# Kernel tuning notes

Measured on AMD Instinct MI355X. Metric: run time of the kernel, lower is better.

## Reference

```python
import jax, jax.numpy as jnp
import numpy as np

B, R, C, H = 2048, 100, 64, 256  # batch graphs, regions/graph, in_channels, hidden
N = B * R                         # total nodes
E = 3276800                       # edges


def setup_inputs() -> dict:
    key = jax.random.key(0)
    ks = jax.random.split(key, 12)
    state = jax.random.normal(ks[0], (N, C), dtype=jnp.float32)
    edge_index = jax.random.randint(ks[1], (2, E), 0, N, dtype=jnp.int64)
    action = jax.random.uniform(ks[2], (B, R, R), dtype=jnp.float32)
    s = lambda f: 1.0 / np.sqrt(f)
    W_gcn = jax.random.uniform(ks[3], (C, C), jnp.float32, -s(C), s(C))
    b_gcn = jnp.zeros((C,), jnp.float32)
    W1 = jax.random.uniform(ks[4], (C + R, H), jnp.float32, -s(C + R), s(C + R))
    b1 = jax.random.uniform(ks[5], (H,), jnp.float32, -s(C + R), s(C + R))
    W2 = jax.random.uniform(ks[6], (H, H), jnp.float32, -s(H), s(H))
    b2 = jax.random.uniform(ks[7], (H,), jnp.float32, -s(H), s(H))
    W3 = jax.random.uniform(ks[8], (H, 1), jnp.float32, -s(H), s(H))
    b3 = jax.random.uniform(ks[9], (1,), jnp.float32, -s(H), s(H))
    return {"state": state, "edge_index": edge_index, "action": action,
            "W_gcn": W_gcn, "b_gcn": b_gcn, "W1": W1, "b1": b1,
            "W2": W2, "b2": b2, "W3": W3, "b3": b3}


def gcn_conv(x, edge_index, W, b):
    # PyG GCNConv: add self-loops, symmetric degree normalization, then aggregate.
    n = x.shape[0]
    loops = jnp.arange(n, dtype=edge_index.dtype)
    src = jnp.concatenate([edge_index[0], loops])
    dst = jnp.concatenate([edge_index[1], loops])
    deg = jax.ops.segment_sum(jnp.ones_like(dst, dtype=x.dtype), dst, num_segments=n)
    dinv = deg ** -0.5  # deg >= 1 thanks to self-loops
    xw = x @ W
    msg = xw[src] * (dinv[src] * dinv[dst])[:, None]
    return jax.ops.segment_sum(msg, dst, num_segments=n) + b


def reference(state, edge_index, action, W_gcn, b_gcn, W1, b1, W2, b2, W3, b3):
    out = jax.nn.relu(gcn_conv(state, edge_index, W_gcn, b_gcn))
    x = out + state                              # residual, [N, C]
    x = x.reshape(-1, R, C)                      # [B, R, C]
    concat = jnp.concatenate([x, action], axis=-1)  # [B, R, C+R]
    x = jax.nn.relu(concat @ W1 + b1)
    x = jax.nn.relu(x @ W2 + b2)
    x = jnp.sum(x, axis=1)                       # sum pooling over regions -> [B, H]
    return (x @ W3 + b3).squeeze(-1)             # [B]
```

## Files before the change

### kernel.cpp

```cpp
#include <hip/hip_runtime.h>
#include <hip/hip_bf16.h>
#include <cstdint>
#include <cstddef>

#define N_NODES 204800
#define N_EDGES 3276800
#define NB 2048
#define NR 100
#define NC 64
#define NH 256
#define KPAD 192
#define NBKT 400
#define H1P 264

typedef __attribute__((ext_vector_type(8))) short short8;
typedef __attribute__((ext_vector_type(4))) float f32x4;
typedef unsigned int uint32;

__device__ __forceinline__ void gload16(const void* g, void* l) {
    __builtin_amdgcn_global_load_lds(
        (const __attribute__((address_space(1))) uint32_t*)(g),
        (__attribute__((address_space(3))) uint32_t*)(l), 16, 0, 0);
}

__device__ __forceinline__ ushort f2bf(float v) {
    __hip_bfloat16 h = __float2bfloat16(v);
    return *reinterpret_cast<ushort*>(&h);
}

__device__ __forceinline__ uint32 pack2bf(float a, float b) {
    return (uint32)f2bf(a) | ((uint32)f2bf(b) << 16);
}

__device__ __forceinline__ float bflo(uint32 v) { return __uint_as_float(v << 16); }
__device__ __forceinline__ float bfhi(uint32 v) { return __uint_as_float(v & 0xFFFF0000u); }


__global__ __launch_bounds__(256) void k_bhist(const int* __restrict__ ei,
                                               int* __restrict__ bcnt) {
    __shared__ int h[NBKT];
    int t = threadIdx.x;
    for (int i = t; i < NBKT; i += 256) h[i] = 0;
    __syncthreads();
    #pragma unroll 8
    for (int k = 0; k < 8; ++k) {
        int e = blockIdx.x * 2048 + k * 256 + t;
        atomicAdd(&h[ei[N_EDGES + e] >> 9], 1);
    }
    __syncthreads();
    for (int i = t; i < NBKT; i += 256)
        if (h[i]) atomicAdd(&bcnt[i], h[i]);
}

__global__ void k_bscan(const int* __restrict__ bcnt, int* __restrict__ boffs,
                        int* __restrict__ bcur) {
    __shared__ int tmp[512];
    int t = threadIdx.x;
    int v = (t < NBKT) ? bcnt[t] : 0;
    tmp[t] = v;
    __syncthreads();
    for (int off = 1; off < 512; off <<= 1) {
        int x = 0;
        if (t >= off) x = tmp[t - off];
        __syncthreads();
        tmp[t] += x;
        __syncthreads();
    }
    if (t < NBKT) {
        int o = tmp[t] - v;
        boffs[t] = o;
        bcur[t] = o;
    }
}

__global__ __launch_bounds__(256) void k_bscat(const int* __restrict__ ei,
                                               int* __restrict__ bcur,
                                               uint32* __restrict__ part) {
    __shared__ int hist[NBKT];
    int tid = threadIdx.x;
    for (int i = tid; i < NBKT; i += 256) hist[i] = 0;
    __syncthreads();

    uint32 w[8];
    int bk[8], r[8];
    #pragma unroll 8
    for (int k = 0; k < 8; ++k) {
        int e = blockIdx.x * 2048 + k * 256 + tid;
        int s = ei[e];
        int d = ei[N_EDGES + e];
        int b = d >> 9;
        w[k] = (uint32)s | ((uint32)(d & 511) << 18);
        bk[k] = b;
        r[k] = atomicAdd(&hist[b], 1);
    }
    __syncthreads();
    for (int i = tid; i < NBKT; i += 256) {
        int c = hist[i];
        hist[i] = c ? atomicAdd(&bcur[i], c) : 0;
    }
    __syncthreads();
    #pragma unroll 8
    for (int k = 0; k < 8; ++k)
        part[hist[bk[k]] + r[k]] = w[k];
}

__global__ __launch_bounds__(512) void k_sortb(
    const uint32* __restrict__ part, const int* __restrict__ boffs,
    const int* __restrict__ bcnt, int* __restrict__ csr,
    int* __restrict__ cnt, int* __restrict__ offs, float* __restrict__ dinv) {
    __shared__ int h[512];
    __shared__ int cur[512];
    int b = blockIdx.x, t = threadIdx.x;
    h[t] = 0;
    __syncthreads();
    int base = boffs[b], n = bcnt[b];
    for (int i = t; i < n; i += 512)
        atomicAdd(&h[part[base + i] >> 18], 1);
    __syncthreads();
    int v = h[t];
    int node = b * 512 + t;
    cnt[node] = v;
    dinv[node] = rsqrtf((float)(v + 1));
    __syncthreads();
    for (int off = 1; off < 512; off <<= 1) {
        int x = 0;
        if (t >= off) x = h[t - off];
        __syncthreads();
        h[t] += x;
        __syncthreads();
    }
    int excl = h[t] - v;
    offs[node] = base + excl;
    cur[t] = excl;
    __syncthreads();
    for (int i = t; i < n; i += 512) {
        uint32 ew = part[base + i];
        int dl = ew >> 18;
        int pos = atomicAdd(&cur[dl], 1);
        csr[base + pos] = (int)(ew & 0x3FFFF);
    }
}

__global__ void k_ssb(const float* __restrict__ state, const float* __restrict__ dinv,
                      uint32* __restrict__ ssb32) {
    int idx = blockIdx.x * 256 + threadIdx.x;
    int row = idx >> 5;
    float d = dinv[row];
    float2 v = reinterpret_cast<const float2*>(state)[idx];
    ssb32[idx] = pack2bf(v.x * d, v.y * d);
}

__global__ __launch_bounds__(256) void k_gcn(
    const uint32* __restrict__ ssb32, const float* __restrict__ state,
    const int* __restrict__ csr, const int* __restrict__ offs,
    const int* __restrict__ cnt, const float* __restrict__ dinv,
    const ushort* __restrict__ Wgt, const float* __restrict__ bg,
    ushort* __restrict__ xb16) {
    __shared__ uint32 av[32 * 36];
    __shared__ ushort wgs[64 * 72];
    int tid = threadIdx.x;
    int w = tid >> 6, lane = tid & 63;
    int half = lane >> 5, l = lane & 31;
    int R0 = blockIdx.x * 32;

    {
        int r = tid >> 2, c0 = (tid & 3) * 16;
        short8 v0 = *(const short8*)(Wgt + r * 64 + c0);
        short8 v1 = *(const short8*)(Wgt + r * 64 + c0 + 8);
        *(short8*)(wgs + r * 72 + c0) = v0;
        *(short8*)(wgs + r * 72 + c0 + 8) = v1;
    }

    for (int rr = 0; rr < 4; ++rr) {
        int lrow = w * 8 + rr * 2 + half;
        int row = R0 + lrow;
        float di = dinv[row];
        float2 st2 = *reinterpret_cast<const float2*>(state + (size_t)row * 64 + 2 * l);
        int s0 = offs[row], c = cnt[row];
        float x0 = 0.f, y0 = 0.f, x1 = 0.f, y1 = 0.f;
        float x2 = 0.f, y2 = 0.f, x3 = 0.f, y3 = 0.f;
        int e = 0;
        for (; e + 8 <= c; e += 8) {
            int sa = csr[s0 + e + 0];
            int sb = csr[s0 + e + 1];
            int sc = csr[s0 + e + 2];
            int sd = csr[s0 + e + 3];
            int se = csr[s0 + e + 4];
            int sf = csr[s0 + e + 5];
            int sg = csr[s0 + e + 6];
            int sh = csr[s0 + e + 7];
            uint32 va = ssb32[(size_t)sa * 32 + l];
            uint32 vb = ssb32[(size_t)sb * 32 + l];
            uint32 vc = ssb32[(size_t)sc * 32 + l];
            uint32 vd = ssb32[(size_t)sd * 32 + l];
            uint32 ve = ssb32[(size_t)se * 32 + l];
            uint32 vf = ssb32[(size_t)sf * 32 + l];
            uint32 vg = ssb32[(size_t)sg * 32 + l];
            uint32 vh = ssb32[(size_t)sh * 32 + l];
            x0 += bflo(va); y0 += bfhi(va);
            x1 += bflo(vb); y1 += bfhi(vb);
            x2 += bflo(vc); y2 += bfhi(vc);
            x3 += bflo(vd); y3 += bfhi(vd);
            x0 += bflo(ve); y0 += bfhi(ve);
            x1 += bflo(vf); y1 += bfhi(vf);
            x2 += bflo(vg); y2 += bfhi(vg);
            x3 += bflo(vh); y3 += bfhi(vh);
        }
        for (; e + 4 <= c; e += 4) {
            int sa = csr[s0 + e + 0];
            int sb = csr[s0 + e + 1];
            int sc = csr[s0 + e + 2];
            int sd = csr[s0 + e + 3];
            uint32 va = ssb32[(size_t)sa * 32 + l];
            uint32 vb = ssb32[(size_t)sb * 32 + l];
            uint32 vc = ssb32[(size_t)sc * 32 + l];
            uint32 vd = ssb32[(size_t)sd * 32 + l];
            x0 += bflo(va); y0 += bfhi(va);
            x1 += bflo(vb); y1 += bfhi(vb);
            x2 += bflo(vc); y2 += bfhi(vc);
            x3 += bflo(vd); y3 += bfhi(vd);
        }
        for (; e < c; ++e) {
            int s = csr[s0 + e];
            uint32 v = ssb32[(size_t)s * 32 + l];
            x0 += bflo(v); y0 += bfhi(v);
        }
        float ax = ((x0 + x1) + (x2 + x3)) * di + di * di * st2.x;
        float ay = ((y0 + y1) + (y2 + y3)) * di + di * di * st2.y;
        av[lrow * 36 + l] = pack2bf(ax, ay);
    }
    __syncthreads();

    int l15 = lane & 15, l4 = lane >> 4;
    const ushort* avs = (const ushort*)av;
    f32x4 acc[2] = {};
    #pragma unroll
    for (int kk = 0; kk < 2; ++kk) {
        short8 bf = *(const short8*)(wgs + (w * 16 + l15) * 72 + kk * 32 + l4 * 8);
        #pragma unroll
        for (int mt = 0; mt < 2; ++mt) {
            short8 af = *(const short8*)(avs + (mt * 16 + l15) * 72 + kk * 32 + l4 * 8);
            acc[mt] = __builtin_amdgcn_mfma_f32_16x16x32_bf16(af, bf, acc[mt], 0, 0, 0);
        }
    }
    int col = w * 16 + l15;
    float bgv = bg[col];
    #pragma unroll
    for (int mt = 0; mt < 2; ++mt)
        #pragma unroll
        for (int r = 0; r < 4; ++r) {
            int row = R0 + mt * 16 + l4 * 4 + r;
            float v = fmaxf(acc[mt][r] + bgv, 0.f) + state[(size_t)row * 64 + col];
            xb16[(size_t)row * 64 + col] = f2bf(v);
        }
}

__global__ void k_packW(const float* __restrict__ W1, const float* __restrict__ W2,
                        const float* __restrict__ Wg, ushort* __restrict__ W1f,
                        ushort* __restrict__ W2f, ushort* __restrict__ Wgt) {
    int t = blockIdx.x * 256 + threadIdx.x;
    if (t < 6 * 4 * 256 * 8) {
        int u = t & 7, chunk = t >> 3;
        int tid = chunk & 255, ktI = chunk >> 8;
        int kt = ktI >> 2, i = ktI & 3;
        int l = tid & 63, wp = tid >> 6;
        int k = kt * 32 + (l >> 4) * 8 + u;
        int j = i * 64 + wp * 16 + (l & 15);
        W1f[t] = (k < NC + NR) ? f2bf(W1[(size_t)k * NH + j]) : (ushort)0;
    } else if (t < 49152 + 8 * 4 * 256 * 8) {
        int t2 = t - 49152;
        int u = t2 & 7, chunk = t2 >> 3;
        int tid = chunk & 255, ktI = chunk >> 8;
        int kt = ktI >> 2, i = ktI & 3;
        int l = tid & 63, wp = tid >> 6;
        int k = kt * 32 + (l >> 4) * 8 + u;
        int j = i * 64 + wp * 16 + (l & 15);
        W2f[t2] = f2bf(W2[(size_t)k * NH + j]);
    } else {
        int t3 = t - 49152 - 65536;
        if (t3 < 64 * 64) {
            int n = t3 >> 6, k = t3 & 63;
            Wgt[t3] = f2bf(Wg[(size_t)k * 64 + n]);
        }
    }
}

__global__ __launch_bounds__(256, 2) void k_mlpf(
    const ushort* __restrict__ xb16, const float* __restrict__ action,
    const ushort* __restrict__ W1f, const ushort* __restrict__ W2f,
    const float* __restrict__ b1, const float* __restrict__ b2,
    const float* __restrict__ W3, float* __restrict__ out) {
    __shared__ __align__(16) ushort As[2][64 * 32];
    __shared__ __align__(16) ushort Bs[2][256 * 32];
    __shared__ __align__(16) ushort H1s[64 * H1P];
    int tid = threadIdx.x;
    int w = tid >> 6, lane = tid & 63;
    int m0 = blockIdx.x * 64;
    int l15 = lane & 15, l4 = lane >> 4;

    int arow = (tid >> 6) * 16 + (tid & 15);
    int aseg = (tid >> 4) & 3;
    int gr = m0 + arow;
    int gb = gr / 100, grr = gr - gb * 100;
    const float* abp = action + (size_t)gb * 10000 + (size_t)grr * 100;

    float b1v[4], b2v[4], w3v[4];
    #pragma unroll
    for (int nt = 0; nt < 4; ++nt) {
        int col = w * 64 + nt * 16 + l15;
        b1v[nt] = b1[col];
        b2v[nt] = b2[col];
        w3v[nt] = W3[col];
    }

    f32x4 acc[4][4] = {};

    #pragma unroll
    for (int i = 0; i < 4; ++i)
        gload16(W1f + ((size_t)(0 * 4 + i) * 256 + tid) * 8, (char*)Bs[0] + i * 4096 + tid * 16);
    gload16(xb16 + (size_t)gr * 64 + 0 * 32 + aseg * 8, (char*)As[0] + tid * 16);
    __syncthreads();

    int cur = 0;
    for (int kt = 0; kt < 6; ++kt) {
        int nxt = cur ^ 1;
        if (kt < 5) {
            #pragma unroll
            for (int i = 0; i < 4; ++i)
                gload16(W1f + ((size_t)((kt + 1) * 4 + i) * 256 + tid) * 8,
                        (char*)Bs[nxt] + i * 4096 + tid * 16);
            if (kt + 1 < 2) {
                gload16(xb16 + (size_t)gr * 64 + (kt + 1) * 32 + aseg * 8,
                        (char*)As[nxt] + tid * 16);
            } else {
                int c0 = (kt + 1) * 32 - 64 + aseg * 8;
                ushort tmp[8];
                #pragma unroll
                for (int u = 0; u < 8; ++u) {
                    int cc = c0 + u;
                    tmp[u] = (cc < NR) ? f2bf(abp[cc]) : (ushort)0;
                }
                *(short8*)((char*)As[nxt] + tid * 16) = *(const short8*)tmp;
            }
        } else {
            #pragma unroll
            for (int i = 0; i < 4; ++i)
                gload16(W2f + ((size_t)(0 * 4 + i) * 256 + tid) * 8,
                        (char*)Bs[nxt] + i * 4096 + tid * 16);
        }
        short8 af[4], bf[4];
        #pragma unroll
        for (int mt = 0; mt < 4; ++mt)
            af[mt] = *(const short8*)((const char*)As[cur] + mt * 1024 + lane * 16);
        #pragma unroll
        for (int nt = 0; nt < 4; ++nt)
            bf[nt] = *(const short8*)((const char*)Bs[cur] + w * 4096 + nt * 1024 + lane * 16);
        #pragma unroll
        for (int mt = 0; mt < 4; ++mt)
            #pragma unroll
            for (int nt = 0; nt < 4; ++nt)
                acc[mt][nt] = __builtin_amdgcn_mfma_f32_16x16x32_bf16(
                    af[mt], bf[nt], acc[mt][nt], 0, 0, 0);
        if (kt == 5) {
            #pragma unroll
            for (int mt = 0; mt < 4; ++mt)
                #pragma unroll
                for (int nt = 0; nt < 4; ++nt) {
                    int col = w * 64 + nt * 16 + l15;
                    #pragma unroll
                    for (int r = 0; r < 4; ++r) {
                        int row = mt * 16 + l4 * 4 + r;
                        H1s[row * H1P + col] = f2bf(fmaxf(acc[mt][nt][r] + b1v[nt], 0.f));
                    }
                }
        }
        __syncthreads();
        cur = nxt;
    }

    #pragma unroll
    for (int mt = 0; mt < 4; ++mt)
        #pragma unroll
        for (int nt = 0; nt < 4; ++nt)
            acc[mt][nt] = (f32x4){0.f, 0.f, 0.f, 0.f};

    for (int kt = 0; kt < 8; ++kt) {
        int nxt = cur ^ 1;
        if (kt < 7) {
            #pragma unroll
            for (int i = 0; i < 4; ++i)
                gload16(W2f + ((size_t)((kt + 1) * 4 + i) * 256 + tid) * 8,
                        (char*)Bs[nxt] + i * 4096 + tid * 16);
        }
        int k0 = kt * 32;
        short8 af[4], bf[4];
        #pragma unroll
        for (int mt = 0; mt < 4; ++mt)
            af[mt] = *(const short8*)((const char*)H1s +
                     ((size_t)(mt * 16 + l15) * H1P + k0 + l4 * 8) * 2);
        #pragma unroll
        for (int nt = 0; nt < 4; ++nt)
            bf[nt] = *(const short8*)((const char*)Bs[cur] + w * 4096 + nt * 1024 + lane * 16);
        #pragma unroll
        for (int mt = 0; mt < 4; ++mt)
            #pragma unroll
            for (int nt = 0; nt < 4; ++nt)
                acc[mt][nt] = __builtin_amdgcn_mfma_f32_16x16x32_bf16(
                    af[mt], bf[nt], acc[mt][nt], 0, 0, 0);
        __syncthreads();
        cur = nxt;
    }

    float* red = (float*)As;
    #pragma unroll
    for (int mt = 0; mt < 4; ++mt)
        #pragma unroll
        for (int r = 0; r < 4; ++r) {
            float v = 0.f;
            #pragma unroll
            for (int nt = 0; nt < 4; ++nt)
                v += fmaxf(acc[mt][nt][r] + b2v[nt], 0.f) * w3v[nt];
            v += __shfl_xor(v, 1);
            v += __shfl_xor(v, 2);
            v += __shfl_xor(v, 4);
            v += __shfl_xor(v, 8);
            if (l15 == 0) red[(mt * 16 + l4 * 4 + r) * 4 + w] = v;
        }
    __syncthreads();
    if (tid < 64) {
        float s = red[tid * 4 + 0] + red[tid * 4 + 1] + red[tid * 4 + 2] + red[tid * 4 + 3];
        int gbase = m0;
        int g0 = gbase / 100;
        int r0 = gbase - g0 * 100;
        int split = 100 - r0; if (split > 64) split = 64;
        float v0 = (tid < split) ? s : 0.f;
        float vs = s;
        #pragma unroll
        for (int d = 1; d < 64; d <<= 1) {
            v0 += __shfl_xor(v0, d);
            vs += __shfl_xor(vs, d);
        }
        if (tid == 0) {
            atomicAdd(&out[g0], v0);
            if (split < 64) atomicAdd(&out[g0 + 1], vs - v0);
        }
    }
}

__global__ void k_init_out(float* __restrict__ out, const float* __restrict__ b3) {
    int i = blockIdx.x * 256 + threadIdx.x;
    out[i] = b3[0];
}


extern "C" void kernel_launch(void* const* d_in, const int* in_sizes, int n_in,
                              void* d_out, int out_size, void* d_ws, size_t ws_size,
                              hipStream_t stream) {
    const float* state  = (const float*)d_in[0];
    const int*   ei     = (const int*)d_in[1];
    const float* action = (const float*)d_in[2];
    const float* Wg     = (const float*)d_in[3];
    const float* bg     = (const float*)d_in[4];
    const float* W1     = (const float*)d_in[5];
    const float* b1     = (const float*)d_in[6];
    const float* W2     = (const float*)d_in[7];
    const float* b2     = (const float*)d_in[8];
    const float* W3     = (const float*)d_in[9];
    const float* b3     = (const float*)d_in[10];
    float* out = (float*)d_out;

    char* ws = (char*)d_ws;
    uint32* part  = (uint32*)(ws + 0);
    uint32* ssb32 = (uint32*)(ws + 13107200);
    ushort* xb16  = (ushort*)(ws + 39321600);
    int*   csr    = (int*)  (ws + 65536000);
    int*   cnt    = (int*)  (ws + 78643200);
    int*   offs   = (int*)  (ws + 79462400);
    float* dinv   = (float*)(ws + 80281600);
    int*   bcnt   = (int*)  (ws + 81100800);
    int*   boffs  = (int*)  (ws + 81102400);
    int*   bcur   = (int*)  (ws + 81104000);
    ushort* W1f   = (ushort*)(ws + 81105600);
    ushort* W2f   = (ushort*)(ws + 81203904);
    ushort* Wgt   = (ushort*)(ws + 81334976);

    hipMemsetAsync(bcnt, 0, NBKT * sizeof(int), stream);
    k_init_out<<<NB / 256, 256, 0, stream>>>(out, b3);

    k_bhist<<<N_EDGES / 2048, 256, 0, stream>>>(ei, bcnt);
    k_bscan<<<1, 512, 0, stream>>>(bcnt, boffs, bcur);
    k_bscat<<<N_EDGES / 2048, 256, 0, stream>>>(ei, bcur, part);
    k_sortb<<<NBKT, 512, 0, stream>>>(part, boffs, bcnt, csr, cnt, offs, dinv);
    k_ssb<<<(N_NODES * 32) / 256, 256, 0, stream>>>(state, dinv, ssb32);
    k_packW<<<(49152 + 65536 + 4096 + 255) / 256, 256, 0, stream>>>(
        W1, W2, Wg, W1f, W2f, Wgt);
    k_gcn<<<N_NODES / 32, 256, 0, stream>>>(ssb32, state, csr, offs, cnt, dinv,
                                            Wgt, bg, xb16);
    k_mlpf<<<N_NODES / 64, 256, 0, stream>>>(xb16, action, W1f, W2f, b1, b2, W3, out);
}
```

Before: 324.7 us.

## Restructure fused MLP to keep activations in registers and fold b1 into W1

Reworks the fused MLP kernel so each wave owns 16 rows and all 256 output columns. It computes a transposed first layer with the row data as the B operand, keeps H1 in registers, and rebuilds the layer-2 A fragments with lane shuffles instead of an LDS H1 buffer. Bias b1 is folded into the packed W1 as an extra K row driven by a constant 1.0 input, and action values are loaded as float4 vectors. Dropping the As/H1s shared buffers cuts LDS so occupancy can rise to 3 blocks, at the cost of higher register pressure (two 16-tile accumulator arrays) and extra shuffle work.

```diff
diff --git a/kernel.cpp b/kernel.cpp
--- a/kernel.cpp
+++ b/kernel.cpp
@@ -11,7 +11,6 @@
 #define NH 256
 #define KPAD 192
 #define NBKT 400
-#define H1P 264
 
 typedef __attribute__((ext_vector_type(8))) short short8;
 typedef __attribute__((ext_vector_type(4))) float f32x4;
@@ -256,8 +255,9 @@
 }
 
 __global__ void k_packW(const float* __restrict__ W1, const float* __restrict__ W2,
-                        const float* __restrict__ Wg, ushort* __restrict__ W1f,
-                        ushort* __restrict__ W2f, ushort* __restrict__ Wgt) {
+                        const float* __restrict__ Wg, const float* __restrict__ b1,
+                        ushort* __restrict__ W1f, ushort* __restrict__ W2f,
+                        ushort* __restrict__ Wgt) {
     int t = blockIdx.x * 256 + threadIdx.x;
     if (t < 6 * 4 * 256 * 8) {
         int u = t & 7, chunk = t >> 3;
@@ -266,7 +266,10 @@
         int l = tid & 63, wp = tid >> 6;
         int k = kt * 32 + (l >> 4) * 8 + u;
         int j = i * 64 + wp * 16 + (l & 15);
-        W1f[t] = (k < NC + NR) ? f2bf(W1[(size_t)k * NH + j]) : (ushort)0;
+        ushort v = 0;
+        if (k < NC + NR) v = f2bf(W1[(size_t)k * NH + j]);
+        else if (k == NC + NR) v = f2bf(b1[j]);
+        W1f[t] = v;
     } else if (t < 49152 + 8 * 4 * 256 * 8) {
         int t2 = t - 49152;
         int u = t2 & 7, chunk = t2 >> 3;
@@ -285,105 +288,95 @@
     }
 }
 
-__global__ __launch_bounds__(256, 2) void k_mlpf(
+__global__ __launch_bounds__(256, 3) void k_mlpf(
     const ushort* __restrict__ xb16, const float* __restrict__ action,
     const ushort* __restrict__ W1f, const ushort* __restrict__ W2f,
-    const float* __restrict__ b1, const float* __restrict__ b2,
-    const float* __restrict__ W3, float* __restrict__ out) {
-    __shared__ __align__(16) ushort As[2][64 * 32];
+    const float* __restrict__ b2, const float* __restrict__ W3,
+    float* __restrict__ out) {
     __shared__ __align__(16) ushort Bs[2][256 * 32];
-    __shared__ __align__(16) ushort H1s[64 * H1P];
     int tid = threadIdx.x;
     int w = tid >> 6, lane = tid & 63;
+    int s = lane & 15, g = lane >> 4;
     int m0 = blockIdx.x * 64;
-    int l15 = lane & 15, l4 = lane >> 4;
-
-    int arow = (tid >> 6) * 16 + (tid & 15);
-    int aseg = (tid >> 4) & 3;
-    int gr = m0 + arow;
-    int gb = gr / 100, grr = gr - gb * 100;
+    int myrow = m0 + w * 16 + s;
+    int gb = myrow / 100, grr = myrow - gb * 100;
     const float* abp = action + (size_t)gb * 10000 + (size_t)grr * 100;
 
-    float b1v[4], b2v[4], w3v[4];
-    #pragma unroll
-    for (int nt = 0; nt < 4; ++nt) {
-        int col = w * 64 + nt * 16 + l15;
-        b1v[nt] = b1[col];
-        b2v[nt] = b2[col];
-        w3v[nt] = W3[col];
-    }
-
-    f32x4 acc[4][4] = {};
+    short8 xf0 = *(const short8*)(xb16 + (size_t)myrow * 64 + g * 8);
+    short8 xf1 = *(const short8*)(xb16 + (size_t)myrow * 64 + 32 + g * 8);
 
     #pragma unroll
     for (int i = 0; i < 4; ++i)
-        gload16(W1f + ((size_t)(0 * 4 + i) * 256 + tid) * 8, (char*)Bs[0] + i * 4096 + tid * 16);
-    gload16(xb16 + (size_t)gr * 64 + 0 * 32 + aseg * 8, (char*)As[0] + tid * 16);
-    __syncthreads();
-
+        gload16(W1f + ((size_t)(0 * 4 + i) * 256 + tid) * 8,
+                (char*)Bs[0] + i * 4096 + tid * 16);
+    __syncthreads();
+
+    f32x4 acc1[16] = {};
+    float4 pa0 = {0.f, 0.f, 0.f, 0.f}, pa1 = {0.f, 0.f, 0.f, 0.f};
     int cur = 0;
+
+    #pragma unroll
     for (int kt = 0; kt < 6; ++kt) {
         int nxt = cur ^ 1;
+        short8 bf;
+        if (kt == 0) bf = xf0;
+        else if (kt == 1) bf = xf1;
+        else if (kt < 5) {
+            ushort tm[8];
+            tm[0] = f2bf(pa0.x); tm[1] = f2bf(pa0.y); tm[2] = f2bf(pa0.z); tm[3] = f2bf(pa0.w);
+            tm[4] = f2bf(pa1.x); tm[5] = f2bf(pa1.y); tm[6] = f2bf(pa1.z); tm[7] = f2bf(pa1.w);
+            bf = *(const short8*)tm;
+        } else {
+            ushort tm[8];
+            if (g == 0) {
+                tm[0] = f2bf(pa0.x); tm[1] = f2bf(pa0.y); tm[2] = f2bf(pa0.z); tm[3] = f2bf(pa0.w);
+                tm[4] = (ushort)0x3F80; tm[5] = 0; tm[6] = 0; tm[7] = 0;
+            } else {
+                #pragma unroll
+                for (int u = 0; u < 8; ++u) tm[u] = 0;
+            }
+            bf = *(const short8*)tm;
+        }
+        if (kt >= 1 && kt <= 3) {
+            int c0 = (kt + 1) * 32 - 64 + g * 8;
+            pa0 = *(const float4*)(abp + c0);
+            pa1 = *(const float4*)(abp + c0 + 4);
+        } else if (kt == 4) {
+            if (g == 0) pa0 = *(const float4*)(abp + 96);
+        }
         if (kt < 5) {
             #pragma unroll
             for (int i = 0; i < 4; ++i)
                 gload16(W1f + ((size_t)((kt + 1) * 4 + i) * 256 + tid) * 8,
                         (char*)Bs[nxt] + i * 4096 + tid * 16);
-            if (kt + 1 < 2) {
-                gload16(xb16 + (size_t)gr * 64 + (kt + 1) * 32 + aseg * 8,
-                        (char*)As[nxt] + tid * 16);
-            } else {
-                int c0 = (kt + 1) * 32 - 64 + aseg * 8;
-                ushort tmp[8];
-                #pragma unroll
-                for (int u = 0; u < 8; ++u) {
-                    int cc = c0 + u;
-                    tmp[u] = (cc < NR) ? f2bf(abp[cc]) : (ushort)0;
-                }
-                *(short8*)((char*)As[nxt] + tid * 16) = *(const short8*)tmp;
-            }
         } else {
             #pragma unroll
             for (int i = 0; i < 4; ++i)
                 gload16(W2f + ((size_t)(0 * 4 + i) * 256 + tid) * 8,
                         (char*)Bs[nxt] + i * 4096 + tid * 16);
         }
-        short8 af[4], bf[4];
         #pragma unroll
-        for (int mt = 0; mt < 4; ++mt)
-            af[mt] = *(const short8*)((const char*)As[cur] + mt * 1024 + lane * 16);
-        #pragma unroll
-        for (int nt = 0; nt < 4; ++nt)
-            bf[nt] = *(const short8*)((const char*)Bs[cur] + w * 4096 + nt * 1024 + lane * 16);
-        #pragma unroll
-        for (int mt = 0; mt < 4; ++mt)
-            #pragma unroll
-            for (int nt = 0; nt < 4; ++nt)
-                acc[mt][nt] = __builtin_amdgcn_mfma_f32_16x16x32_bf16(
-                    af[mt], bf[nt], acc[mt][nt], 0, 0, 0);
-        if (kt == 5) {
-            #pragma unroll
-            for (int mt = 0; mt < 4; ++mt)
-                #pragma unroll
-                for (int nt = 0; nt < 4; ++nt) {
-                    int col = w * 64 + nt * 16 + l15;
-                    #pragma unroll
-                    for (int r = 0; r < 4; ++r) {
-                        int row = mt * 16 + l4 * 4 + r;
-                        H1s[row * H1P + col] = f2bf(fmaxf(acc[mt][nt][r] + b1v[nt], 0.f));
-                    }
-                }
+        for (int jt = 0; jt < 16; ++jt) {
+            short8 af = *(const short8*)((const char*)Bs[cur] +
+                         (jt >> 2) * 4096 + (jt & 3) * 1024 + lane * 16);
+            acc1[jt] = __builtin_amdgcn_mfma_f32_16x16x32_bf16(af, bf, acc1[jt], 0, 0, 0);
         }
         __syncthreads();
         cur = nxt;
     }
 
-    #pragma unroll
-    for (int mt = 0; mt < 4; ++mt)
-        #pragma unroll
-        for (int nt = 0; nt < 4; ++nt)
-            acc[mt][nt] = (f32x4){0.f, 0.f, 0.f, 0.f};
-
+    uint32 q0[16], q1[16];
+    #pragma unroll
+    for (int jt = 0; jt < 16; ++jt) {
+        q0[jt] = pack2bf(fmaxf(acc1[jt][0], 0.f), fmaxf(acc1[jt][1], 0.f));
+        q1[jt] = pack2bf(fmaxf(acc1[jt][2], 0.f), fmaxf(acc1[jt][3], 0.f));
+    }
+
+    f32x4 acc2[16] = {};
+    int src0 = ((lane & 16) << 1) | s;
+    int src1 = src0 + 16;
+    bool hiSel = (lane & 32) != 0;
+    #pragma unroll
     for (int kt = 0; kt < 8; ++kt) {
         int nxt = cur ^ 1;
         if (kt < 7) {
@@ -392,49 +385,58 @@
                 gload16(W2f + ((size_t)((kt + 1) * 4 + i) * 256 + tid) * 8,
                         (char*)Bs[nxt] + i * 4096 + tid * 16);
         }
-        int k0 = kt * 32;
-        short8 af[4], bf[4];
+        uint32 al0 = (uint32)__shfl((int)q0[2 * kt],     src0);
+        uint32 ah0 = (uint32)__shfl((int)q0[2 * kt + 1], src0);
+        uint32 bl0 = (uint32)__shfl((int)q1[2 * kt],     src0);
+        uint32 bh0 = (uint32)__shfl((int)q1[2 * kt + 1], src0);
+        uint32 al1 = (uint32)__shfl((int)q0[2 * kt],     src1);
+        uint32 ah1 = (uint32)__shfl((int)q0[2 * kt + 1], src1);
+        uint32 bl1 = (uint32)__shfl((int)q1[2 * kt],     src1);
+        uint32 bh1 = (uint32)__shfl((int)q1[2 * kt + 1], src1);
+        short8 af;
+        uint32* afp = (uint32*)&af;
+        afp[0] = hiSel ? ah0 : al0;
+        afp[1] = hiSel ? bh0 : bl0;
+        afp[2] = hiSel ? ah1 : al1;
+        afp[3] = hiSel ? bh1 : bl1;
         #pragma unroll
-        for (int mt = 0; mt < 4; ++mt)
-            af[mt] = *(const short8*)((const char*)H1s +
-                     ((size_t)(mt * 16 + l15) * H1P + k0 + l4 * 8) * 2);
-        #pragma unroll
-        for (int nt = 0; nt < 4; ++nt)
-            bf[nt] = *(const short8*)((const char*)Bs[cur] + w * 4096 + nt * 1024 + lane * 16);
-        #pragma unroll
-        for (int mt = 0; mt < 4; ++mt)
-            #pragma unroll
-            for (int nt = 0; nt < 4; ++nt)
-                acc[mt][nt] = __builtin_amdgcn_mfma_f32_16x16x32_bf16(
-                    af[mt], bf[nt], acc[mt][nt], 0, 0, 0);
+        for (int nt = 0; nt < 16; ++nt) {
+            short8 bf = *(const short8*)((const char*)Bs[cur] +
+                         (nt >> 2) * 4096 + (nt & 3) * 1024 + lane * 16);
+            acc2[nt] = __builtin_amdgcn_mfma_f32_16x16x32_bf16(af, bf, acc2[nt], 0, 0, 0);
+        }
         __syncthreads();
         cur = nxt;
     }
 
-    float* red = (float*)As;
-    #pragma unroll
-    for (int mt = 0; mt < 4; ++mt)
+    float vsum[4] = {0.f, 0.f, 0.f, 0.f};
+    #pragma unroll
+    for (int nt = 0; nt < 16; ++nt) {
+        float b2v = b2[nt * 16 + s];
+        float w3v = W3[nt * 16 + s];
         #pragma unroll
-        for (int r = 0; r < 4; ++r) {
-            float v = 0.f;
-            #pragma unroll
-            for (int nt = 0; nt < 4; ++nt)
-                v += fmaxf(acc[mt][nt][r] + b2v[nt], 0.f) * w3v[nt];
-            v += __shfl_xor(v, 1);
-            v += __shfl_xor(v, 2);
-            v += __shfl_xor(v, 4);
-            v += __shfl_xor(v, 8);
-            if (l15 == 0) red[(mt * 16 + l4 * 4 + r) * 4 + w] = v;
-        }
+        for (int r = 0; r < 4; ++r)
+            vsum[r] += fmaxf(acc2[nt][r] + b2v, 0.f) * w3v;
+    }
+    float* red = (float*)Bs;
+    #pragma unroll
+    for (int r = 0; r < 4; ++r) {
+        float v = vsum[r];
+        v += __shfl_xor(v, 1);
+        v += __shfl_xor(v, 2);
+        v += __shfl_xor(v, 4);
+        v += __shfl_xor(v, 8);
+        if (s == 0) red[w * 16 + g * 4 + r] = v;
+    }
     __syncthreads();
     if (tid < 64) {
-        float s = red[tid * 4 + 0] + red[tid * 4 + 1] + red[tid * 4 + 2] + red[tid * 4 + 3];
+        float sv = red[tid];
         int gbase = m0;
         int g0 = gbase / 100;
         int r0 = gbase - g0 * 100;
         int split = 100 - r0; if (split > 64) split = 64;
-        float v0 = (tid < split) ? s : 0.f;
-        float vs = s;
+        float v0 = (tid < split) ? sv : 0.f;
+        float vs = sv;
         #pragma unroll
         for (int d = 1; d < 64; d <<= 1) {
             v0 += __shfl_xor(v0, d);
@@ -493,8 +495,8 @@
     k_sortb<<<NBKT, 512, 0, stream>>>(part, boffs, bcnt, csr, cnt, offs, dinv);
     k_ssb<<<(N_NODES * 32) / 256, 256, 0, stream>>>(state, dinv, ssb32);
     k_packW<<<(49152 + 65536 + 4096 + 255) / 256, 256, 0, stream>>>(
-        W1, W2, Wg, W1f, W2f, Wgt);
+        W1, W2, Wg, b1, W1f, W2f, Wgt);
     k_gcn<<<N_NODES / 32, 256, 0, stream>>>(ssb32, state, csr, offs, cnt, dinv,
                                             Wgt, bg, xb16);
-    k_mlpf<<<N_NODES / 64, 256, 0, stream>>>(xb16, action, W1f, W2f, b1, b2, W3, out);
-}
+    k_mlpf<<<N_NODES / 64, 256, 0, stream>>>(xb16, action, W1f, W2f, b2, W3, out);
+}
```

After: 303.0 us. 1.07x faster.
